# Optimization experiments

Measured on AMD Instinct MI355X. Metric: run time of the kernel, lower is better.

The kernel has to match this reference:

```python
import jax, jax.numpy as jnp
import numpy as np

D = 1024
H = 16
HD = D // H
COND = 128
MLP = 4 * D
B, S = 4, 1024
LN_EPS = 1e-5


def _layer_norm(x, w):
    # fp32 LayerNorm (no bias), then scale by weight, matching custom LayerNorm
    xf = x.astype(jnp.float32)
    mu = jnp.mean(xf, axis=-1, keepdims=True)
    var = jnp.mean(jnp.square(xf - mu), axis=-1, keepdims=True)
    y = (xf - mu) * jax.lax.rsqrt(var + LN_EPS)
    return y * w[None, None, :]


def _modulate(x, shift, scale):
    # shift/scale: [B, D] -> broadcast over seq
    return x * (1.0 + scale[:, None, :]) + shift[:, None, :]


def _rope(t, cos, sin):
    # t: [B,S,H,hd]; cos/sin: [S, hd//2]  (GPT-NeoX half-split rotary)
    c = cos[None, :, None, :]
    s = sin[None, :, None, :]
    t1, t2 = jnp.split(t, 2, axis=-1)
    return jnp.concatenate([t1 * c - t2 * s, t2 * c + t1 * s], axis=-1)


def setup_inputs() -> dict:
    key = jax.random.key(0)
    ks = jax.random.split(key, 12)
    std = 0.02
    inp = {
        "x": jax.random.normal(ks[0], (B, S, D), dtype=jnp.float32),
        "c": jax.random.normal(ks[1], (B, COND), dtype=jnp.float32),
        "norm1_w": jnp.ones((D,), dtype=jnp.float32),
        "norm2_w": jnp.ones((D,), dtype=jnp.float32),
        "w_qkv": jax.random.normal(ks[2], (D, 3 * D), dtype=jnp.float32) * std,
        "w_out": jax.random.normal(ks[3], (D, D), dtype=jnp.float32) * std,
        "w1": jax.random.normal(ks[4], (D, MLP), dtype=jnp.float32) * std,
        "b1": jnp.zeros((MLP,), dtype=jnp.float32),
        "w2": jax.random.normal(ks[5], (MLP, D), dtype=jnp.float32) * std,
        "b2": jnp.zeros((D,), dtype=jnp.float32),
        "adaLN_w": jax.random.normal(ks[6], (COND, 6 * D), dtype=jnp.float32) * std,
        "adaLN_b": jnp.zeros((6 * D,), dtype=jnp.float32),
    }
    # rotary tables: cos/sin [S, hd//2]
    inv_freq = 1.0 / (10000.0 ** (jnp.arange(0, HD, 2, dtype=jnp.float32) / HD))
    t = jnp.arange(S, dtype=jnp.float32)
    freqs = t[:, None] * inv_freq[None, :]  # [S, hd//2]
    inp["cos"] = jnp.cos(freqs)
    inp["sin"] = jnp.sin(freqs)
    return inp


def reference(x, c, norm1_w, norm2_w, w_qkv, w_out, w1, b1, w2, b2, adaLN_w, adaLN_b, cos, sin):
    b, s, d = x.shape
    hd = 2 * cos.shape[-1]
    h = d // hd

    # adaLN modulation -> 6 chunks of [B, D]
    mod = c @ adaLN_w + adaLN_b
    shift_msa, scale_msa, gate_msa, shift_mlp, scale_mlp, gate_mlp = jnp.split(mod, 6, axis=-1)

    x_skip = x
    xm = _modulate(_layer_norm(x, norm1_w), shift_msa, scale_msa)

    qkv = (xm @ w_qkv).reshape(b, s, 3, h, hd)
    q = _rope(qkv[:, :, 0], cos, sin)
    k = _rope(qkv[:, :, 1], cos, sin)
    v = qkv[:, :, 2]

    scale = 1.0 / jnp.sqrt(jnp.asarray(hd, dtype=x.dtype))
    scores = jnp.einsum("bshd,bthd->bhst", q, k) * scale
    probs = jax.nn.softmax(scores, axis=-1)
    attn = jnp.einsum("bhst,bthd->bshd", probs, v).reshape(b, s, d)

    # bias_dropout_add_scale (inference: dropout off): residual + gate * out
    x = x_skip + gate_msa[:, None, :] * (attn @ w_out)

    xm2 = _modulate(_layer_norm(x, norm2_w), shift_mlp, scale_mlp)
    hdn = jax.nn.gelu(xm2 @ w1 + b1, approximate=True)
    mlp_out = hdn @ w2 + b2
    x = x + gate_mlp[:, None, :] * mlp_out
    return x
```

## Files before the change

kernel.cpp:

```cpp
#include <hip/hip_runtime.h>

typedef unsigned short u16;
typedef unsigned int u32;
typedef short bf16x8 __attribute__((ext_vector_type(8)));
typedef float f32x4 __attribute__((ext_vector_type(4)));

#define DD 1024
#define SS 1024
#define HH 16
#define HDIM 64
#define MODW 6144

__device__ __forceinline__ float b2f(u16 h){ u32 u = ((u32)h)<<16; return __builtin_bit_cast(float,u); }
__device__ __forceinline__ u16 f2b(float f){
  u32 u = __builtin_bit_cast(u32,f);
  return (u16)((u + 0x7fffu + ((u>>16)&1u))>>16);
}
__device__ __forceinline__ void gload16(const u16* g, u16* l){
  __builtin_amdgcn_global_load_lds((const __attribute__((address_space(1))) void*)g,
                                   (__attribute__((address_space(3))) void*)l, 16, 0, 0);
}

__global__ void k_zero(float* __restrict__ out){
  int i = blockIdx.x*256 + threadIdx.x;
  ((float4*)out)[i] = make_float4(0.f,0.f,0.f,0.f);
}

__device__ __forceinline__ void tcast_tile(const float* in, u16* out, int K, int N, int bx, int by){
  __shared__ float t[32][33];
  int n0 = bx*32, k0 = by*32;
  int tx = threadIdx.x & 31, ty = threadIdx.x >> 5;
  #pragma unroll
  for (int i=0;i<4;i++){
    int k = k0 + ty + i*8;
    t[ty+i*8][tx] = in[(size_t)k*N + n0 + tx];
  }
  __syncthreads();
  #pragma unroll
  for (int i=0;i<4;i++){
    int n = n0 + ty + i*8;
    out[(size_t)n*K + k0 + tx] = f2b(t[tx][ty+i*8]);
  }
}
__global__ void k_prep(const float* __restrict__ wqkv, const float* __restrict__ wout,
                       const float* __restrict__ w1, const float* __restrict__ w2,
                       u16* __restrict__ wqkvT, u16* __restrict__ woutT,
                       u16* __restrict__ w1T, u16* __restrict__ w2T,
                       const float* __restrict__ c, const float* __restrict__ aw,
                       const float* __restrict__ ab, float* __restrict__ mod){
  int bid = blockIdx.x;
  if (bid < 3072)       tcast_tile(wqkv, wqkvT, 1024, 3072, bid%96,  bid/96);
  else if (bid < 4096){ int t=bid-3072; tcast_tile(wout, woutT, 1024, 1024, t%32, t/32); }
  else if (bid < 8192){ int t=bid-4096; tcast_tile(w1,   w1T,   1024, 4096, t%128,t/128); }
  else if (bid < 12288){int t=bid-8192; tcast_tile(w2,   w2T,   4096, 1024, t%32, t/32); }
  else {
    int t = bid - 12288;
    int n = (t%24)*256 + threadIdx.x;
    int bb = t/24;
    float acc = ab[n];
    #pragma unroll 4
    for (int k=0;k<128;k++) acc += c[bb*128+k]*aw[(size_t)k*MODW + n];
    mod[(size_t)bb*MODW + n] = acc;
  }
}

__global__ void k_ln_mod(const float* __restrict__ x, const float* __restrict__ w,
                         const float* __restrict__ mod, int shc, int scc,
                         u16* __restrict__ out){
  int row = blockIdx.x;
  int b = row >> 10;
  const float* xr = x + (size_t)row*DD;
  float4 v = ((const float4*)xr)[threadIdx.x];
  float s = v.x+v.y+v.z+v.w;
  float sq = v.x*v.x+v.y*v.y+v.z*v.z+v.w*v.w;
  #pragma unroll
  for (int o=32;o;o>>=1){ s += __shfl_xor(s,o); sq += __shfl_xor(sq,o); }
  __shared__ float ls[4], lq[4];
  int wid = threadIdx.x>>6, lane = threadIdx.x&63;
  if (lane==0){ ls[wid]=s; lq[wid]=sq; }
  __syncthreads();
  s = ls[0]+ls[1]+ls[2]+ls[3]; sq = lq[0]+lq[1]+lq[2]+lq[3];
  float mu = s*(1.f/DD);
  float var = sq*(1.f/DD) - mu*mu;
  float rs = rsqrtf(var + 1e-5f);
  int d0 = threadIdx.x*4;
  const float* mb = mod + (size_t)b*MODW;
  float y0 = ((v.x-mu)*rs*w[d0+0])*(1.f+mb[scc+d0+0]) + mb[shc+d0+0];
  float y1 = ((v.y-mu)*rs*w[d0+1])*(1.f+mb[scc+d0+1]) + mb[shc+d0+1];
  float y2 = ((v.z-mu)*rs*w[d0+2])*(1.f+mb[scc+d0+2]) + mb[shc+d0+2];
  float y3 = ((v.w-mu)*rs*w[d0+3])*(1.f+mb[scc+d0+3]) + mb[shc+d0+3];
  uint2 pk;
  pk.x = (u32)f2b(y0) | ((u32)f2b(y1)<<16);
  pk.y = (u32)f2b(y2) | ((u32)f2b(y3)<<16);
  ((uint2*)(out + (size_t)row*DD))[threadIdx.x] = pk;
}

enum { EPI_QKV=0, EPI_GELU=2, EPI_PARTB=5 };

template<int EPI>
__launch_bounds__(512, 6)
__global__ void k_gemm(const u16* __restrict__ A, const u16* __restrict__ Bt,
                       int M, int N, int K, int kstride,
                       const float* __restrict__ bias,
                       float* __restrict__ outf, u16* __restrict__ outb,
                       const float* __restrict__ cosb, const float* __restrict__ sinb,
                       u16* __restrict__ qh, u16* __restrict__ kh, u16* __restrict__ vt){
  __shared__ __align__(16) u16 As[8192], Bs[8192];
  int tid = threadIdx.x, lane = tid & 63;
  int wid = tid >> 6;
  int wr = wid >> 2, wc = wid & 3;
  int nf0 = (wc & 1) + ((wc >> 1) << 2);
  int bm = blockIdx.x*128, bn = blockIdx.y*128;
  int z = blockIdx.z;
  f32x4 acc[4][2] = {};
  int r0 = ((tid>>6)<<4)|(tid&15), c0 = ((tid>>4)&3)<<3;
  const u16* pa0 = A  + (size_t)(bm+r0)*kstride + (size_t)z*K + c0;
  const u16* pb0 = Bt + (size_t)(bn+r0)*kstride + (size_t)z*K + c0;
  int nk = K>>6;
  for (int kt=0; kt<nk; ++kt){
    __syncthreads();
    gload16(pa0,    As + tid*8);  gload16(pa0+32, As + (512+tid)*8);
    gload16(pb0,    Bs + tid*8);  gload16(pb0+32, Bs + (512+tid)*8);
    pa0 += 64; pb0 += 64;
    __syncthreads();
    #pragma unroll
    for (int ch=0; ch<2; ++ch){
      bf16x8 fa[4], fb[2];
      #pragma unroll
      for (int i=0;i<4;i++) fa[i] = *(const bf16x8*)(As + (ch*512 + (wr*4+i)*64 + lane)*8);
      #pragma unroll
      for (int i=0;i<2;i++) fb[i] = *(const bf16x8*)(Bs + (ch*512 + (nf0+2*i)*64 + lane)*8);
      #pragma unroll
      for (int mi=0;mi<4;mi++)
        #pragma unroll
        for (int ni=0;ni<2;ni++)
          acc[mi][ni] = __builtin_amdgcn_mfma_f32_16x16x32_bf16(fa[mi], fb[ni], acc[mi][ni], 0,0,0);
    }
  }
  int rb = bm + wr*64 + ((lane>>4)<<2);
  int ln = lane & 15;
  if (EPI == EPI_QKV){
    int cbg = bn + (wc>>1)*64;
    int ii = cbg >> 10;
    int hh = (cbg >> 6) & 15;
    int dlow = (wc&1)*16 + ln;
    if (ii == 2){
      #pragma unroll
      for (int mi=0;mi<4;mi++){
        int row = rb + mi*16;
        int s = row & 1023, b = row >> 10;
        size_t ob = (size_t)(b*16+hh)*65536;
        #pragma unroll
        for (int i=0;i<2;i++){
          int d = dlow + i*32;
          u32 lo = (u32)f2b(acc[mi][i][0]) | ((u32)f2b(acc[mi][i][1])<<16);
          u32 hi = (u32)f2b(acc[mi][i][2]) | ((u32)f2b(acc[mi][i][3])<<16);
          *(uint2*)(vt + ob + (size_t)d*1024 + s) = make_uint2(lo,hi);
        }
      }
    } else {
      u16* dst = (ii==0) ? qh : kh;
      #pragma unroll
      for (int mi=0;mi<4;mi++){
        #pragma unroll
        for (int r=0;r<4;r++){
          int row = rb + mi*16 + r;
          int s = row & 1023, b = row >> 10;
          size_t ob = ((size_t)(b*16+hh)*1024 + s)*64;
          float cc = cosb[s*32 + dlow], sn = sinb[s*32 + dlow];
          float t1 = acc[mi][0][r], t2 = acc[mi][1][r];
          dst[ob + dlow]      = f2b(t1*cc - t2*sn);
          dst[ob + dlow + 32] = f2b(t2*cc + t1*sn);
        }
      }
    }
    return;
  }
  if (EPI == EPI_PARTB){
    u16* po = outb + (size_t)z*M*N;
    #pragma unroll
    for (int mi=0;mi<4;mi++)
      #pragma unroll
      for (int ni=0;ni<2;ni++){
        int col = bn + (nf0+2*ni)*16 + ln;
        #pragma unroll
        for (int r=0;r<4;r++)
          po[(size_t)(rb+mi*16+r)*N + col] = f2b(acc[mi][ni][r]);
      }
    return;
  }
  #pragma unroll
  for (int mi=0;mi<4;mi++){
    #pragma unroll
    for (int ni=0;ni<2;ni++){
      int col = bn + (nf0+2*ni)*16 + ln;
      #pragma unroll
      for (int r=0;r<4;r++){
        int row = rb + mi*16 + r;
        float t = acc[mi][ni][r] + bias[col];
        float y = 0.7978845608f*(t + 0.044715f*t*t*t);
        y = fminf(fmaxf(y, -15.f), 15.f);
        float e = __expf(2.f*y);
        float g = 0.5f*t*(1.f + (e-1.f)/(e+1.f));
        outb[(size_t)row*N + col] = f2b(g);
      }
    }
  }
}

__global__ void k_red_ln(const u16* __restrict__ part, const float* __restrict__ x,
                         const float* __restrict__ mod, const float* __restrict__ w,
                         float* __restrict__ x2, u16* __restrict__ act){
  int row = blockIdx.x;
  int b = row >> 10;
  int tid = threadIdx.x;
  int col = tid*4;
  size_t base = (size_t)row*DD + col;
  const size_t MN = (size_t)4096*1024;
  uint2 p0 = *(const uint2*)(part + base);
  uint2 p1 = *(const uint2*)(part + MN + base);
  const float* mb = mod + (size_t)b*MODW;
  float4 g = *(const float4*)(mb + 2*DD + col);
  float4 rr = *(const float4*)(x + base);
  float4 v;
  v.x = rr.x + g.x*(b2f((u16)p0.x)      + b2f((u16)p1.x));
  v.y = rr.y + g.y*(b2f((u16)(p0.x>>16))+ b2f((u16)(p1.x>>16)));
  v.z = rr.z + g.z*(b2f((u16)p0.y)      + b2f((u16)p1.y));
  v.w = rr.w + g.w*(b2f((u16)(p0.y>>16))+ b2f((u16)(p1.y>>16)));
  *(float4*)(x2 + base) = v;
  float s = v.x+v.y+v.z+v.w;
  float sq = v.x*v.x+v.y*v.y+v.z*v.z+v.w*v.w;
  #pragma unroll
  for (int o=32;o;o>>=1){ s += __shfl_xor(s,o); sq += __shfl_xor(sq,o); }
  __shared__ float ls[4], lq[4];
  int wid = tid>>6, lane = tid&63;
  if (lane==0){ ls[wid]=s; lq[wid]=sq; }
  __syncthreads();
  s = ls[0]+ls[1]+ls[2]+ls[3]; sq = lq[0]+lq[1]+lq[2]+lq[3];
  float mu = s*(1.f/DD);
  float var = sq*(1.f/DD) - mu*mu;
  float rs = rsqrtf(var + 1e-5f);
  float y0 = ((v.x-mu)*rs*w[col+0])*(1.f+mb[4*DD+col+0]) + mb[3*DD+col+0];
  float y1 = ((v.y-mu)*rs*w[col+1])*(1.f+mb[4*DD+col+1]) + mb[3*DD+col+1];
  float y2 = ((v.z-mu)*rs*w[col+2])*(1.f+mb[4*DD+col+2]) + mb[3*DD+col+2];
  float y3 = ((v.w-mu)*rs*w[col+3])*(1.f+mb[4*DD+col+3]) + mb[3*DD+col+3];
  uint2 pk;
  pk.x = (u32)f2b(y0) | ((u32)f2b(y1)<<16);
  pk.y = (u32)f2b(y2) | ((u32)f2b(y3)<<16);
  *(uint2*)(act + base) = pk;
}

__global__ void k_reduce4b(const u16* __restrict__ part, size_t MN,
                           const float* __restrict__ resid,
                           const float* __restrict__ mod, int gate_off,
                           const float* __restrict__ bias,
                           float* __restrict__ out){
  int i = blockIdx.x*256 + threadIdx.x;
  int e = i<<2;
  int col = e & 1023;
  int row = e >> 10;
  int b = row >> 10;
  float4 s = make_float4(0.f,0.f,0.f,0.f);
  #pragma unroll
  for (int z=0; z<4; z++){
    uint2 p = ((const uint2*)(part + (size_t)z*MN))[i];
    s.x += b2f((u16)p.x); s.y += b2f((u16)(p.x>>16));
    s.z += b2f((u16)p.y); s.w += b2f((u16)(p.y>>16));
  }
  float4 bb = *(const float4*)(bias + col);
  s.x+=bb.x; s.y+=bb.y; s.z+=bb.z; s.w+=bb.w;
  float4 g = *(const float4*)(mod + (size_t)b*MODW + gate_off + col);
  float4 rr = ((const float4*)resid)[i];
  float4 o;
  o.x = rr.x + g.x*s.x; o.y = rr.y + g.y*s.y;
  o.z = rr.z + g.z*s.z; o.w = rr.w + g.w*s.w;
  ((float4*)out)[i] = o;
}

__launch_bounds__(256)
__global__ void k_attn(const u16* __restrict__ qh, const u16* __restrict__ kh,
                       const u16* __restrict__ vt, u16* __restrict__ attn){
  int blk = blockIdx.x;
  int bh = blk >> 4;
  int qt = blk & 15;
  int tid = threadIdx.x, lane = tid&63, wid = tid>>6;
  int ln = lane&15, kg = lane>>4;
  __shared__ __align__(16) u16 Ks[64*72];
  __shared__ __align__(16) u16 Vs[64*72];
  __shared__ __align__(16) float ps[4][16*72];
  const size_t hb = (size_t)bh*SS*HDIM;

  int qrow = qt*64 + wid*16 + ln;
  const u16* qp = qh + hb + (size_t)qrow*64 + kg*8;
  bf16x8 qf0 = *(const bf16x8*)qp;
  bf16x8 qf1 = *(const bf16x8*)(qp + 32);

  float m[4], l[4];
  f32x4 oc[4] = {};
  #pragma unroll
  for (int r=0;r<4;r++){ m[r]=-1e30f; l[r]=0.f; }
  float* psw = ps[wid];

  for (int kt=0; kt<16; ++kt){
    __syncthreads();
    {
      int row = tid>>2, c = tid&3;
      const u16* gk = kh + hb + (size_t)(kt*64+row)*64 + c*16;
      *(uint4*)(Ks + row*72 + c*16)     = *(const uint4*)gk;
      *(uint4*)(Ks + row*72 + c*16 + 8) = *(const uint4*)(gk+8);
      const u16* gv = vt + hb + (size_t)row*1024 + kt*64 + c*16;
      *(uint4*)(Vs + row*72 + c*16)     = *(const uint4*)gv;
      *(uint4*)(Vs + row*72 + c*16 + 8) = *(const uint4*)(gv+8);
    }
    __syncthreads();

    f32x4 sc[4] = {};
    #pragma unroll
    for (int c=0;c<4;c++){
      bf16x8 kf0 = *(const bf16x8*)(Ks + (c*16+ln)*72 + kg*8);
      bf16x8 kf1 = *(const bf16x8*)(Ks + (c*16+ln)*72 + kg*8 + 32);
      sc[c] = __builtin_amdgcn_mfma_f32_16x16x32_bf16(qf0, kf0, sc[c], 0,0,0);
      sc[c] = __builtin_amdgcn_mfma_f32_16x16x32_bf16(qf1, kf1, sc[c], 0,0,0);
    }
    #pragma unroll
    for (int r=0;r<4;r++){
      float s0 = sc[0][r]*0.125f, s1 = sc[1][r]*0.125f;
      float s2 = sc[2][r]*0.125f, s3 = sc[3][r]*0.125f;
      float mx = fmaxf(fmaxf(s0,s1), fmaxf(s2,s3));
      #pragma unroll
      for (int off=8;off;off>>=1) mx = fmaxf(mx, __shfl_xor(mx, off));
      float mn = fmaxf(m[r], mx);
      float al = __expf(m[r]-mn);
      m[r] = mn;
      float p0=__expf(s0-mn), p1=__expf(s1-mn), p2=__expf(s2-mn), p3=__expf(s3-mn);
      float sum = (p0+p1)+(p2+p3);
      #pragma unroll
      for (int off=8;off;off>>=1) sum += __shfl_xor(sum, off);
      l[r] = l[r]*al + sum;
      #pragma unroll
      for (int c=0;c<4;c++) oc[c][r] *= al;
      int ro = (kg*4+r)*72;
      psw[ro +  0 + ln] = p0;
      psw[ro + 16 + ln] = p1;
      psw[ro + 32 + ln] = p2;
      psw[ro + 48 + ln] = p3;
    }
    #pragma unroll
    for (int kc=0; kc<2; ++kc){
      const float* pr = psw + ln*72 + kg*8 + kc*32;
      f32x4 a0 = *(const f32x4*)pr;
      f32x4 a1 = *(const f32x4*)(pr+4);
      bf16x8 af;
      af[0]=f2b(a0[0]); af[1]=f2b(a0[1]); af[2]=f2b(a0[2]); af[3]=f2b(a0[3]);
      af[4]=f2b(a1[0]); af[5]=f2b(a1[1]); af[6]=f2b(a1[2]); af[7]=f2b(a1[3]);
      #pragma unroll
      for (int c=0;c<4;c++){
        bf16x8 vf = *(const bf16x8*)(Vs + (c*16+ln)*72 + kg*8 + kc*32);
        oc[c] = __builtin_amdgcn_mfma_f32_16x16x32_bf16(af, vf, oc[c], 0,0,0);
      }
    }
  }
  int b = bh >> 4, h = bh & 15;
  #pragma unroll
  for (int r=0;r<4;r++){
    int srow = qt*64 + wid*16 + kg*4 + r;
    float inv = 1.f/l[r];
    u16* op = attn + (size_t)(b*1024+srow)*DD + h*64;
    #pragma unroll
    for (int c=0;c<4;c++) op[c*16+ln] = f2b(oc[c][r]*inv);
  }
}

extern "C" void kernel_launch(void* const* d_in, const int* in_sizes, int n_in,
                              void* d_out, int out_size, void* d_ws, size_t ws_size,
                              hipStream_t stream){
  const float* x   = (const float*)d_in[0];
  const float* c   = (const float*)d_in[1];
  const float* n1w = (const float*)d_in[2];
  const float* n2w = (const float*)d_in[3];
  const float* wqkv= (const float*)d_in[4];
  const float* wout= (const float*)d_in[5];
  const float* w1  = (const float*)d_in[6];
  const float* b1  = (const float*)d_in[7];
  const float* w2  = (const float*)d_in[8];
  const float* b2  = (const float*)d_in[9];
  const float* aw  = (const float*)d_in[10];
  const float* ab  = (const float*)d_in[11];
  const float* cosb= (const float*)d_in[12];
  const float* sinb= (const float*)d_in[13];

  const size_t REQ = 117538816;
  if (ws_size < REQ){
    k_zero<<<4096,256,0,stream>>>((float*)d_out);
    return;
  }
  char* ws = (char*)d_ws;
  u16*   wqkvT = (u16*)(ws + 0);
  u16*   woutT = (u16*)(ws + 6291456);
  u16*   act   = (u16*)(ws + 8388608);
  float* mod   = (float*)(ws + 16777216);
  float* x2    = (float*)(ws + 16875520);
  u16*   qh    = (u16*)(ws + 16875520);
  u16*   kh    = (u16*)(ws + 25264128);
  u16*   vt    = (u16*)(ws + 33652736);
  u16*   part2b= (u16*)(ws + 33652736);
  u16*   hbuf  = (u16*)(ws + 33652736);
  u16*   w1T   = (u16*)(ws + 67207168);
  u16*   w2T   = (u16*)(ws + 75595776);
  u16*   part4b= (u16*)(ws + 83984384);

  k_prep<<<12384,256,0,stream>>>(wqkv, wout, w1, w2, wqkvT, woutT, w1T, w2T, c, aw, ab, mod);
  k_ln_mod<<<4096,256,0,stream>>>(x, n1w, mod, 0*DD, 1*DD, act);
  k_gemm<EPI_QKV ><<<dim3(32,24,1),512,0,stream>>>(act, wqkvT, 4096,3072,1024,1024,
        nullptr, nullptr, nullptr, cosb, sinb, qh, kh, vt);
  k_attn<<<1024,256,0,stream>>>(qh, kh, vt, act);
  k_gemm<EPI_PARTB><<<dim3(32,8,2),512,0,stream>>>(act, woutT, 4096,1024,512,1024,
        nullptr, nullptr, part2b, nullptr, nullptr, nullptr, nullptr, nullptr);
  k_red_ln<<<4096,256,0,stream>>>(part2b, x, mod, n2w, x2, act);
  k_gemm<EPI_GELU><<<dim3(32,32,1),512,0,stream>>>(act, w1T, 4096,4096,1024,1024,
        b1, nullptr, hbuf, nullptr, nullptr, nullptr, nullptr, nullptr);
  k_gemm<EPI_PARTB><<<dim3(32,8,4),512,0,stream>>>(hbuf, w2T, 4096,1024,1024,4096,
        nullptr, nullptr, part4b, nullptr, nullptr, nullptr, nullptr, nullptr);
  k_reduce4b<<<4096,256,0,stream>>>(part4b, (size_t)4096*1024, x2, mod, 5*DD, b2, (float*)d_out);
}
```

Before: 437.8 us.

## Use 256x256 GEMM tiles with a 4-stage async LDS pipeline

Replaces the 128x128 GEMM with a 256x256-tile kernel where each wave computes 128x64. Global-to-LDS loads are issued three K-steps ahead into a 4-slot ring buffer, with explicit vmcnt waits and raised priority around the MFMA block. This aims to increase operand reuse and hide global load latency. The trade-off is fewer blocks (some grids fall below the CU count), larger LDS use and higher register pressure.

```diff
diff --git a/kernel.cpp b/kernel.cpp
--- a/kernel.cpp
+++ b/kernel.cpp
@@ -98,79 +98,98 @@
 enum { EPI_QKV=0, EPI_GELU=2, EPI_PARTB=5 };
 
 template<int EPI>
-__launch_bounds__(512, 6)
-__global__ void k_gemm(const u16* __restrict__ A, const u16* __restrict__ Bt,
-                       int M, int N, int K, int kstride,
-                       const float* __restrict__ bias,
-                       float* __restrict__ outf, u16* __restrict__ outb,
-                       const float* __restrict__ cosb, const float* __restrict__ sinb,
-                       u16* __restrict__ qh, u16* __restrict__ kh, u16* __restrict__ vt){
-  __shared__ __align__(16) u16 As[8192], Bs[8192];
+__launch_bounds__(512, 2)
+__global__ void k_gemm256(const u16* __restrict__ A, const u16* __restrict__ Bt,
+                          int M, int N, int K, int kstride,
+                          const float* __restrict__ bias,
+                          u16* __restrict__ outb,
+                          const float* __restrict__ cosb, const float* __restrict__ sinb,
+                          u16* __restrict__ qh, u16* __restrict__ kh, u16* __restrict__ vt){
+  __shared__ __align__(16) u16 lds[4][2][8192];
   int tid = threadIdx.x, lane = tid & 63;
-  int wid = tid >> 6;
-  int wr = wid >> 2, wc = wid & 3;
-  int nf0 = (wc & 1) + ((wc >> 1) << 2);
-  int bm = blockIdx.x*128, bn = blockIdx.y*128;
-  int z = blockIdx.z;
-  f32x4 acc[4][2] = {};
-  int r0 = ((tid>>6)<<4)|(tid&15), c0 = ((tid>>4)&3)<<3;
-  const u16* pa0 = A  + (size_t)(bm+r0)*kstride + (size_t)z*K + c0;
-  const u16* pb0 = Bt + (size_t)(bn+r0)*kstride + (size_t)z*K + c0;
-  int nk = K>>6;
-  for (int kt=0; kt<nk; ++kt){
-    __syncthreads();
-    gload16(pa0,    As + tid*8);  gload16(pa0+32, As + (512+tid)*8);
-    gload16(pb0,    Bs + tid*8);  gload16(pb0+32, Bs + (512+tid)*8);
-    pa0 += 64; pb0 += 64;
-    __syncthreads();
-    #pragma unroll
-    for (int ch=0; ch<2; ++ch){
-      bf16x8 fa[4], fb[2];
-      #pragma unroll
-      for (int i=0;i<4;i++) fa[i] = *(const bf16x8*)(As + (ch*512 + (wr*4+i)*64 + lane)*8);
-      #pragma unroll
-      for (int i=0;i<2;i++) fb[i] = *(const bf16x8*)(Bs + (ch*512 + (nf0+2*i)*64 + lane)*8);
-      #pragma unroll
-      for (int mi=0;mi<4;mi++)
-        #pragma unroll
-        for (int ni=0;ni<2;ni++)
-          acc[mi][ni] = __builtin_amdgcn_mfma_f32_16x16x32_bf16(fa[mi], fb[ni], acc[mi][ni], 0,0,0);
-    }
-  }
-  int rb = bm + wr*64 + ((lane>>4)<<2);
+  int wid = tid >> 6, wr = wid >> 2, wc = wid & 3;
+  int bm = blockIdx.x*256, bn = blockIdx.y*256, z = blockIdx.z;
+  f32x4 acc[8][4] = {};
+  int srow = (tid>>6)*16 + (tid&15);
+  int skk  = ((tid>>4)&3)*8;
+  const u16* pa = A  + (size_t)(bm+srow)*kstride + (size_t)z*K + skk;
+  const u16* pb = Bt + (size_t)(bn+srow)*kstride + (size_t)z*K + skk;
+  size_t rh = (size_t)128*kstride;
+  int nk = K >> 5;
+  #pragma unroll
+  for (int t=0; t<3; ++t){
+    gload16(pa + t*32,      &lds[t][0][tid*8]);
+    gload16(pa + rh + t*32, &lds[t][0][4096 + tid*8]);
+    gload16(pb + t*32,      &lds[t][1][tid*8]);
+    gload16(pb + rh + t*32, &lds[t][1][4096 + tid*8]);
+  }
+  for (int t=0; t<nk; ++t){
+    const u16* lA = &lds[t&3][0][0];
+    const u16* lB = &lds[t&3][1][0];
+    int ahead = nk-1-t;
+    if (ahead >= 2)      asm volatile("s_waitcnt vmcnt(8)" ::: "memory");
+    else if (ahead == 1) asm volatile("s_waitcnt vmcnt(4)" ::: "memory");
+    else                 asm volatile("s_waitcnt vmcnt(0)" ::: "memory");
+    __builtin_amdgcn_s_barrier();
+    if (t+3 < nk){
+      int u = t+3;
+      gload16(pa + u*32,      &lds[u&3][0][tid*8]);
+      gload16(pa + rh + u*32, &lds[u&3][0][4096 + tid*8]);
+      gload16(pb + u*32,      &lds[u&3][1][tid*8]);
+      gload16(pb + rh + u*32, &lds[u&3][1][4096 + tid*8]);
+    }
+    bf16x8 fa[8], fb[4];
+    #pragma unroll
+    for (int mi=0;mi<8;mi++) fa[mi] = *(const bf16x8*)(lA + ((wr*8+mi)*64 + lane)*8);
+    #pragma unroll
+    for (int ni=0;ni<4;ni++) fb[ni] = *(const bf16x8*)(lB + ((wc*4+ni)*64 + lane)*8);
+    asm volatile("s_waitcnt lgkmcnt(0)" ::: "memory");
+    __builtin_amdgcn_sched_barrier(0);
+    __builtin_amdgcn_s_setprio(1);
+    #pragma unroll
+    for (int mi=0;mi<8;mi++)
+      #pragma unroll
+      for (int ni=0;ni<4;ni++)
+        acc[mi][ni] = __builtin_amdgcn_mfma_f32_16x16x32_bf16(fa[mi], fb[ni], acc[mi][ni], 0,0,0);
+    __builtin_amdgcn_s_setprio(0);
+  }
   int ln = lane & 15;
+  int rbase = bm + wr*128 + ((lane>>4)<<2);
   if (EPI == EPI_QKV){
-    int cbg = bn + (wc>>1)*64;
+    int cbg = bn + wc*64;
     int ii = cbg >> 10;
     int hh = (cbg >> 6) & 15;
-    int dlow = (wc&1)*16 + ln;
     if (ii == 2){
       #pragma unroll
-      for (int mi=0;mi<4;mi++){
-        int row = rb + mi*16;
+      for (int mi=0;mi<8;mi++){
+        int row = rbase + mi*16;
         int s = row & 1023, b = row >> 10;
         size_t ob = (size_t)(b*16+hh)*65536;
         #pragma unroll
-        for (int i=0;i<2;i++){
-          int d = dlow + i*32;
-          u32 lo = (u32)f2b(acc[mi][i][0]) | ((u32)f2b(acc[mi][i][1])<<16);
-          u32 hi = (u32)f2b(acc[mi][i][2]) | ((u32)f2b(acc[mi][i][3])<<16);
+        for (int ni=0;ni<4;ni++){
+          int d = ni*16 + ln;
+          u32 lo = (u32)f2b(acc[mi][ni][0]) | ((u32)f2b(acc[mi][ni][1])<<16);
+          u32 hi = (u32)f2b(acc[mi][ni][2]) | ((u32)f2b(acc[mi][ni][3])<<16);
           *(uint2*)(vt + ob + (size_t)d*1024 + s) = make_uint2(lo,hi);
         }
       }
     } else {
       u16* dst = (ii==0) ? qh : kh;
       #pragma unroll
-      for (int mi=0;mi<4;mi++){
+      for (int mi=0;mi<8;mi++){
         #pragma unroll
         for (int r=0;r<4;r++){
-          int row = rb + mi*16 + r;
+          int row = rbase + mi*16 + r;
           int s = row & 1023, b = row >> 10;
           size_t ob = ((size_t)(b*16+hh)*1024 + s)*64;
-          float cc = cosb[s*32 + dlow], sn = sinb[s*32 + dlow];
-          float t1 = acc[mi][0][r], t2 = acc[mi][1][r];
-          dst[ob + dlow]      = f2b(t1*cc - t2*sn);
-          dst[ob + dlow + 32] = f2b(t2*cc + t1*sn);
+          #pragma unroll
+          for (int ni=0;ni<2;ni++){
+            int dlow = ni*16 + ln;
+            float cc = cosb[s*32 + dlow], sn = sinb[s*32 + dlow];
+            float t1 = acc[mi][ni][r], t2 = acc[mi][ni+2][r];
+            dst[ob + dlow]      = f2b(t1*cc - t2*sn);
+            dst[ob + dlow + 32] = f2b(t2*cc + t1*sn);
+          }
         }
       }
     }
@@ -179,33 +198,32 @@
   if (EPI == EPI_PARTB){
     u16* po = outb + (size_t)z*M*N;
     #pragma unroll
-    for (int mi=0;mi<4;mi++)
-      #pragma unroll
-      for (int ni=0;ni<2;ni++){
-        int col = bn + (nf0+2*ni)*16 + ln;
+    for (int mi=0;mi<8;mi++)
+      #pragma unroll
+      for (int ni=0;ni<4;ni++){
+        int col = bn + wc*64 + ni*16 + ln;
         #pragma unroll
         for (int r=0;r<4;r++)
-          po[(size_t)(rb+mi*16+r)*N + col] = f2b(acc[mi][ni][r]);
+          po[(size_t)(rbase+mi*16+r)*N + col] = f2b(acc[mi][ni][r]);
       }
     return;
   }
   #pragma unroll
-  for (int mi=0;mi<4;mi++){
-    #pragma unroll
-    for (int ni=0;ni<2;ni++){
-      int col = bn + (nf0+2*ni)*16 + ln;
+  for (int mi=0;mi<8;mi++)
+    #pragma unroll
+    for (int ni=0;ni<4;ni++){
+      int col = bn + wc*64 + ni*16 + ln;
+      float bb = bias[col];
       #pragma unroll
       for (int r=0;r<4;r++){
-        int row = rb + mi*16 + r;
-        float t = acc[mi][ni][r] + bias[col];
+        float t = acc[mi][ni][r] + bb;
         float y = 0.7978845608f*(t + 0.044715f*t*t*t);
         y = fminf(fmaxf(y, -15.f), 15.f);
         float e = __expf(2.f*y);
         float g = 0.5f*t*(1.f + (e-1.f)/(e+1.f));
-        outb[(size_t)row*N + col] = f2b(g);
+        outb[(size_t)(rbase+mi*16+r)*N + col] = f2b(g);
       }
     }
-  }
 }
 
 __global__ void k_red_ln(const u16* __restrict__ part, const float* __restrict__ x,
@@ -411,15 +429,15 @@
 
   k_prep<<<12384,256,0,stream>>>(wqkv, wout, w1, w2, wqkvT, woutT, w1T, w2T, c, aw, ab, mod);
   k_ln_mod<<<4096,256,0,stream>>>(x, n1w, mod, 0*DD, 1*DD, act);
-  k_gemm<EPI_QKV ><<<dim3(32,24,1),512,0,stream>>>(act, wqkvT, 4096,3072,1024,1024,
-        nullptr, nullptr, nullptr, cosb, sinb, qh, kh, vt);
+  k_gemm256<EPI_QKV ><<<dim3(16,12,1),512,0,stream>>>(act, wqkvT, 4096,3072,1024,1024,
+        nullptr, nullptr, cosb, sinb, qh, kh, vt);
   k_attn<<<1024,256,0,stream>>>(qh, kh, vt, act);
-  k_gemm<EPI_PARTB><<<dim3(32,8,2),512,0,stream>>>(act, woutT, 4096,1024,512,1024,
-        nullptr, nullptr, part2b, nullptr, nullptr, nullptr, nullptr, nullptr);
+  k_gemm256<EPI_PARTB><<<dim3(16,4,2),512,0,stream>>>(act, woutT, 4096,1024,512,1024,
+        nullptr, part2b, nullptr, nullptr, nullptr, nullptr, nullptr);
   k_red_ln<<<4096,256,0,stream>>>(part2b, x, mod, n2w, x2, act);
-  k_gemm<EPI_GELU><<<dim3(32,32,1),512,0,stream>>>(act, w1T, 4096,4096,1024,1024,
-        b1, nullptr, hbuf, nullptr, nullptr, nullptr, nullptr, nullptr);
-  k_gemm<EPI_PARTB><<<dim3(32,8,4),512,0,stream>>>(hbuf, w2T, 4096,1024,1024,4096,
-        nullptr, nullptr, part4b, nullptr, nullptr, nullptr, nullptr, nullptr);
+  k_gemm256<EPI_GELU><<<dim3(16,16,1),512,0,stream>>>(act, w1T, 4096,4096,1024,1024,
+        b1, hbuf, nullptr, nullptr, nullptr, nullptr, nullptr);
+  k_gemm256<EPI_PARTB><<<dim3(16,4,4),512,0,stream>>>(hbuf, w2T, 4096,1024,1024,4096,
+        nullptr, part4b, nullptr, nullptr, nullptr, nullptr, nullptr);
   k_reduce4b<<<4096,256,0,stream>>>(part4b, (size_t)4096*1024, x2, mod, 5*DD, b2, (float*)d_out);
 }
```

After: 377.5 us. 1.16x faster.
